# Kernel optimization log

Measured on AMD Instinct MI355X. Metric: run time of the kernel, lower is better.

## Reference

```python
import jax, jax.numpy as jnp
import numpy as np

DIM = 768
HEADS = 12
HD = DIM // HEADS
SCALE = HD ** -0.5


def setup_inputs() -> dict:
    key = jax.random.key(0)
    ks = jax.random.split(key, 12)
    B, N = 2, 2048
    s = DIM ** -0.5
    return {
        "x1": jax.random.normal(ks[0], (B, N, DIM), jnp.float32),
        "x2": jax.random.normal(ks[1], (B, N, DIM), jnp.float32),
        "Wq": jax.random.normal(ks[2], (DIM, DIM), jnp.float32) * s,
        "bq": jax.random.normal(ks[3], (DIM,), jnp.float32) * 0.01,
        "Wk": jax.random.normal(ks[4], (DIM, DIM), jnp.float32) * s,
        "bk": jax.random.normal(ks[5], (DIM,), jnp.float32) * 0.01,
        "Wv": jax.random.normal(ks[6], (DIM, DIM), jnp.float32) * s,
        "bv": jax.random.normal(ks[7], (DIM,), jnp.float32) * 0.01,
        "Wo": jax.random.normal(ks[8], (DIM, DIM), jnp.float32) * s,
        "bo": jax.random.normal(ks[9], (DIM,), jnp.float32) * 0.01,
        "cross_scale": jnp.array([0.5], jnp.float32),
    }


def _heads(x, W, b):
    # torch Linear: x @ W.T + b; then (B,N,H,hd) -> (B,H,N,hd)
    B, N, _ = x.shape
    y = x @ W.T + b
    return y.reshape(B, N, HEADS, HD).transpose(0, 2, 1, 3)


def reference(x1, x2, Wq, bq, Wk, bk, Wv, bv, Wo, bo, cross_scale):
    B, N, C = x1.shape
    q1, k1, v1 = _heads(x1, Wq, bq), _heads(x1, Wk, bk), _heads(x1, Wv, bv)
    q2, k2, v2 = _heads(x2, Wq, bq), _heads(x2, Wk, bk), _heads(x2, Wv, bv)

    s = cross_scale[0]
    attn11 = jnp.einsum('bhqd,bhkd->bhqk', q1, k1) * SCALE
    attn22 = jnp.einsum('bhqd,bhkd->bhqk', q2, k2) * SCALE
    attn12 = jnp.einsum('bhqd,bhkd->bhqk', q1, k2) * SCALE
    attn21 = jnp.einsum('bhqd,bhkd->bhqk', q2, k1) * SCALE

    a1 = jax.nn.softmax((1.0 - s) * attn11 + s * attn12, axis=-1)
    a2 = jax.nn.softmax((1.0 - s) * attn22 + s * attn21, axis=-1)

    o1 = jnp.einsum('bhqk,bhkd->bhqd', a1, v1).transpose(0, 2, 1, 3).reshape(B, N, C)
    o2 = jnp.einsum('bhqk,bhkd->bhqd', a2, v2).transpose(0, 2, 1, 3).reshape(B, N, C)

    out1 = o1 @ Wo.T + bo
    out2 = o2 @ Wo.T + bo
    return out1, out2
```

## Files before the change

kernel.cpp:

```cpp
#include <hip/hip_runtime.h>

#define KDIM 768
#define HALF 3145728
#define XAELEMS 6291456
#define WELEMS 589824
#define QS 0.18033688f

typedef __attribute__((ext_vector_type(8))) short short8;
typedef __attribute__((ext_vector_type(4))) float float4_;

__device__ __forceinline__ unsigned short f2bf(float f) {
  unsigned int u = __float_as_uint(f);
  u += 0x7fffu + ((u >> 16) & 1u);
  return (unsigned short)(u >> 16);
}

__device__ __forceinline__ void gll16(const void* g, void* l) {
  __builtin_amdgcn_global_load_lds(
      (const __attribute__((address_space(1))) unsigned int*)g,
      (__attribute__((address_space(3))) unsigned int*)l, 16, 0, 0);
}

__global__ void prep_x_kernel(const float* __restrict__ x1, const float* __restrict__ x2,
                              const float* __restrict__ cs,
                              unsigned short* __restrict__ xa, unsigned short* __restrict__ xb) {
  const int i = (blockIdx.x * 256 + threadIdx.x) * 4;
  const float s = cs[0], t_ = 1.0f - s;
  float4 a = *(const float4*)(x1 + i);
  float4 b = *(const float4*)(x2 + i);
  ushort4 ua = { f2bf(a.x), f2bf(a.y), f2bf(a.z), f2bf(a.w) };
  ushort4 ub = { f2bf(b.x), f2bf(b.y), f2bf(b.z), f2bf(b.w) };
  *(ushort4*)(xa + i) = ua;
  *(ushort4*)(xa + HALF + i) = ub;
  ushort4 c1 = { f2bf(t_*a.x + s*b.x), f2bf(t_*a.y + s*b.y), f2bf(t_*a.z + s*b.z), f2bf(t_*a.w + s*b.w) };
  ushort4 c2 = { f2bf(t_*b.x + s*a.x), f2bf(t_*b.y + s*a.y), f2bf(t_*b.z + s*a.z), f2bf(t_*b.w + s*a.w) };
  *(ushort4*)(xb + i) = c1;
  *(ushort4*)(xb + HALF + i) = c2;
}

__global__ void conv_w4_kernel(const float* __restrict__ w0, const float* __restrict__ w1,
                               const float* __restrict__ w2, const float* __restrict__ w3,
                               unsigned short* __restrict__ o0, unsigned short* __restrict__ o1,
                               unsigned short* __restrict__ o2, unsigned short* __restrict__ o3) {
  const int z = blockIdx.y;
  const float* w = (z == 0) ? w0 : (z == 1) ? w1 : (z == 2) ? w2 : w3;
  unsigned short* o = (z == 0) ? o0 : (z == 1) ? o1 : (z == 2) ? o2 : o3;
  const int i = (blockIdx.x * 256 + threadIdx.x) * 4;
  float4 a = *(const float4*)(w + i);
  ushort4 ua = { f2bf(a.x), f2bf(a.y), f2bf(a.z), f2bf(a.w) };
  *(ushort4*)(o + i) = ua;
}

__device__ __forceinline__ void gemm_mainloop(const unsigned short* __restrict__ A,
                                              const unsigned short* __restrict__ W,
                                              unsigned short* As, unsigned short* Bs,
                                              int m0, int n0, int t, float4_ (&acc)[4][4]) {
  const int lane = t & 63, quad = lane >> 4, lrow = lane & 15;
  const int wave = t >> 6;
  const int wm = (wave & 1) * 64, wn = (wave >> 1) * 64;
  for (int kt = 0; kt < KDIM; kt += 64) {
#pragma unroll
    for (int i = 0; i < 4; i++) {
      const int li = i * 256 + t;
      const int row = li >> 3, cc = (li & 7) * 8;
      gll16(A + (size_t)(m0 + row) * KDIM + kt + cc, As + li * 8);
      gll16(W + (size_t)(n0 + row) * KDIM + kt + cc, Bs + li * 8);
    }
    __syncthreads();
#pragma unroll
    for (int kk = 0; kk < 2; kk++) {
      short8 af[4], bfr[4];
#pragma unroll
      for (int i = 0; i < 4; i++)
        af[i] = *(const short8*)(As + (wm + i * 16 + lrow) * 64 + kk * 32 + quad * 8);
#pragma unroll
      for (int j = 0; j < 4; j++)
        bfr[j] = *(const short8*)(Bs + (wn + j * 16 + lrow) * 64 + kk * 32 + quad * 8);
#pragma unroll
      for (int i = 0; i < 4; i++)
#pragma unroll
        for (int j = 0; j < 4; j++)
          acc[i][j] = __builtin_amdgcn_mfma_f32_16x16x32_bf16(af[i], bfr[j], acc[i][j], 0, 0, 0);
    }
    __syncthreads();
  }
}

__global__ __launch_bounds__(256, 2)
void qkv_gemm(const unsigned short* __restrict__ xa, const unsigned short* __restrict__ xb,
              const unsigned short* __restrict__ wq, const unsigned short* __restrict__ wk,
              const unsigned short* __restrict__ wv,
              const float* __restrict__ bq, const float* __restrict__ bk, const float* __restrict__ bv,
              unsigned short* __restrict__ qo, unsigned short* __restrict__ ko,
              unsigned short* __restrict__ vto) {
  __shared__ __align__(16) unsigned short smem[16384];
  unsigned short* As = smem;
  unsigned short* Bs = smem + 8192;
  const int t = threadIdx.x;
  const int z = blockIdx.z;
  const int m0 = blockIdx.x * 128, n0 = blockIdx.y * 128;
  const unsigned short* A = (z == 1) ? xb : xa;
  const unsigned short* W = (z == 0) ? wq : (z == 1) ? wk : wv;
  const float* bias = (z == 0) ? bq : (z == 1) ? bk : bv;
  float4_ acc[4][4];
#pragma unroll
  for (int i = 0; i < 4; i++)
#pragma unroll
    for (int j = 0; j < 4; j++) acc[i][j] = (float4_){0.f, 0.f, 0.f, 0.f};
  gemm_mainloop(A, W, As, Bs, m0, n0, t, acc);

  const int lane = t & 63, quad = lane >> 4, lrow = lane & 15;
  const int wave = t >> 6;
  const int wm = (wave & 1) * 64, wn = (wave >> 1) * 64;

  if (z == 2) {
    unsigned short* Tb = smem + wave * 4096;
#pragma unroll
    for (int i = 0; i < 4; i++) {
#pragma unroll
      for (int j = 0; j < 4; j++) {
        const int nl = j * 16 + lrow;
        const float bn = bias[n0 + wn + nl];
#pragma unroll
        for (int r = 0; r < 4; r++) {
          const int ml = i * 16 + quad * 4 + r;
          const int c = ml >> 3;
          Tb[nl * 64 + ((c ^ (nl & 7)) * 8) + (ml & 7)] = f2bf(acc[i][j][r] + bn);
        }
      }
    }
    __asm__ __volatile__("s_waitcnt lgkmcnt(0)");
    const int sb = (m0 + wm) >> 11;
    const int hh = (n0 + wn) >> 6;
    const int tokbase = ((m0 + wm) & 2047);
#pragma unroll
    for (int i3 = 0; i3 < 8; i3++) {
      const int ci = i3 * 64 + lane;
      const int row = ci >> 3, p = ci & 7;
      short8 rd = *(const short8*)(Tb + row * 64 + p * 8);
      const int c = p ^ (row & 7);
      *(short8*)(vto + ((size_t)(sb * 12 + hh) * 64 + row) * 2048 + tokbase + c * 8) = rd;
    }
  } else {
    unsigned short* dst = (z == 0) ? qo : ko;
    const float scale = (z == 0) ? QS : 1.0f;
#pragma unroll
    for (int i = 0; i < 4; i++) {
#pragma unroll
      for (int j = 0; j < 4; j++) {
        const int n = n0 + wn + j * 16 + lrow;
        const float bn = bias[n];
#pragma unroll
        for (int r = 0; r < 4; r++) {
          const int m = m0 + wm + i * 16 + quad * 4 + r;
          dst[(size_t)m * KDIM + n] = f2bf((acc[i][j][r] + bn) * scale);
        }
      }
    }
  }
}

__global__ __launch_bounds__(256, 2)
void out_gemm(const unsigned short* __restrict__ ob, const unsigned short* __restrict__ wo,
              const float* __restrict__ bo, float* __restrict__ out) {
  __shared__ __align__(16) unsigned short As[128 * 64];
  __shared__ __align__(16) unsigned short Bs[128 * 64];
  const int t = threadIdx.x;
  const int m0 = blockIdx.x * 128, n0 = blockIdx.y * 128;
  float4_ acc[4][4];
#pragma unroll
  for (int i = 0; i < 4; i++)
#pragma unroll
    for (int j = 0; j < 4; j++) acc[i][j] = (float4_){0.f, 0.f, 0.f, 0.f};
  gemm_mainloop(ob, wo, As, Bs, m0, n0, t, acc);

  const int lane = t & 63, quad = lane >> 4, lrow = lane & 15;
  const int wave = t >> 6;
  const int wm = (wave & 1) * 64, wn = (wave >> 1) * 64;
#pragma unroll
  for (int i = 0; i < 4; i++) {
#pragma unroll
    for (int j = 0; j < 4; j++) {
      const int n = n0 + wn + j * 16 + lrow;
      const float bn = bo[n];
#pragma unroll
      for (int r = 0; r < 4; r++) {
        const int m = m0 + wm + i * 16 + quad * 4 + r;
        out[(size_t)m * KDIM + n] = acc[i][j][r] + bn;
      }
    }
  }
}

__global__ __launch_bounds__(256, 2)
void attn_kernel(const unsigned short* __restrict__ qg, const unsigned short* __restrict__ kg,
                 const unsigned short* __restrict__ vt, unsigned short* __restrict__ o) {
  __shared__ __align__(16) unsigned short Ks[2][64 * 64];
  __shared__ __align__(16) unsigned short Vs[2][64 * 64];
  __shared__ __align__(16) unsigned short Ps[4][32 * 72];
  const int prob = blockIdx.x >> 4;
  const int q0 = (blockIdx.x & 15) * 128;
  const int sb = prob / 12, h = prob % 12;
  const int t = threadIdx.x, w = t >> 6, lane = t & 63, quad = lane >> 4, lrow = lane & 15;
  const int mbase = sb * 2048;
  const size_t vbase = (size_t)prob * (64 * 2048);

  short8 aq[2][2];
#pragma unroll
  for (int i = 0; i < 2; i++) {
    const unsigned short* qp = qg + (size_t)(mbase + q0 + w * 32 + i * 16 + lrow) * KDIM + h * 64 + quad * 8;
    aq[i][0] = *(const short8*)qp;
    aq[i][1] = *(const short8*)(qp + 32);
  }
  float l_part[2][4] = {{0.f, 0.f, 0.f, 0.f}, {0.f, 0.f, 0.f, 0.f}};
  float4_ oa[2][4];
#pragma unroll
  for (int i = 0; i < 2; i++)
#pragma unroll
    for (int d = 0; d < 4; d++) oa[i][d] = (float4_){0.f, 0.f, 0.f, 0.f};

  auto stage = [&](int k0, int b) {
#pragma unroll
    for (int i2 = 0; i2 < 2; i2++) {
      const int li = i2 * 256 + t;
      const int row = li >> 3, p = li & 7;
      const int c = p ^ (row & 7);
      gll16(kg + (size_t)(mbase + k0 + row) * KDIM + h * 64 + c * 8, &Ks[b][li * 8]);
    }
#pragma unroll
    for (int i2 = 0; i2 < 2; i2++) {
      const int li = i2 * 256 + t;
      const int row = li >> 3, p = li & 7;
      const int c = p ^ (row & 7);
      gll16(vt + vbase + (size_t)row * 2048 + k0 + c * 8, &Vs[b][li * 8]);
    }
  };
  stage(0, 0);

  for (int kt = 0; kt < 32; kt++) {
    __syncthreads();
    const int b = kt & 1;
    if (kt + 1 < 32) stage((kt + 1) * 64, b ^ 1);

    float4_ sc[2][4];
#pragma unroll
    for (int i = 0; i < 2; i++)
#pragma unroll
      for (int nt = 0; nt < 4; nt++) sc[i][nt] = (float4_){0.f, 0.f, 0.f, 0.f};
#pragma unroll
    for (int kk = 0; kk < 2; kk++) {
#pragma unroll
      for (int nt = 0; nt < 4; nt++) {
        short8 bk_ = *(const short8*)(&Ks[b][(nt * 16 + lrow) * 64 + (((kk * 4 + quad) ^ (lrow & 7)) * 8)]);
        sc[0][nt] = __builtin_amdgcn_mfma_f32_16x16x32_bf16(aq[0][kk], bk_, sc[0][nt], 0, 0, 0);
        sc[1][nt] = __builtin_amdgcn_mfma_f32_16x16x32_bf16(aq[1][kk], bk_, sc[1][nt], 0, 0, 0);
      }
    }

    unsigned short* pw = &Ps[w][0];
#pragma unroll
    for (int i = 0; i < 2; i++)
#pragma unroll
      for (int nt = 0; nt < 4; nt++)
#pragma unroll
        for (int r = 0; r < 4; r++) {
          const float p = __builtin_amdgcn_exp2f(sc[i][nt][r]);
          l_part[i][r] += p;
          pw[(i * 16 + quad * 4 + r) * 72 + nt * 16 + lrow] = f2bf(p);
        }
    __asm__ __volatile__("s_waitcnt lgkmcnt(0)");

#pragma unroll
    for (int kk = 0; kk < 2; kk++) {
      short8 ap0 = *(const short8*)(pw + (0 * 16 + lrow) * 72 + kk * 32 + quad * 8);
      short8 ap1 = *(const short8*)(pw + (1 * 16 + lrow) * 72 + kk * 32 + quad * 8);
#pragma unroll
      for (int dt = 0; dt < 4; dt++) {
        short8 bv_ = *(const short8*)(&Vs[b][(dt * 16 + lrow) * 64 + (((kk * 4 + quad) ^ (lrow & 7)) * 8)]);
        oa[0][dt] = __builtin_amdgcn_mfma_f32_16x16x32_bf16(ap0, bv_, oa[0][dt], 0, 0, 0);
        oa[1][dt] = __builtin_amdgcn_mfma_f32_16x16x32_bf16(ap1, bv_, oa[1][dt], 0, 0, 0);
      }
    }
  }

#pragma unroll
  for (int i = 0; i < 2; i++) {
#pragma unroll
    for (int r = 0; r < 4; r++) {
      float l = l_part[i][r];
      l += __shfl_xor(l, 1);
      l += __shfl_xor(l, 2);
      l += __shfl_xor(l, 4);
      l += __shfl_xor(l, 8);
      const float inv = 1.0f / l;
      const size_t m = (size_t)mbase + q0 + w * 32 + i * 16 + quad * 4 + r;
#pragma unroll
      for (int dt = 0; dt < 4; dt++)
        o[m * KDIM + h * 64 + dt * 16 + lrow] = f2bf(oa[i][dt][r] * inv);
    }
  }
}

extern "C" void kernel_launch(void* const* d_in, const int* in_sizes, int n_in,
                              void* d_out, int out_size, void* d_ws, size_t ws_size,
                              hipStream_t stream) {
  const float* x1 = (const float*)d_in[0];
  const float* x2 = (const float*)d_in[1];
  const float* Wq = (const float*)d_in[2];
  const float* bq = (const float*)d_in[3];
  const float* Wk = (const float*)d_in[4];
  const float* bk = (const float*)d_in[5];
  const float* Wv = (const float*)d_in[6];
  const float* bv = (const float*)d_in[7];
  const float* Wo = (const float*)d_in[8];
  const float* bo = (const float*)d_in[9];
  const float* cs = (const float*)d_in[10];
  float* out = (float*)d_out;

  char* ws = (char*)d_ws;
  size_t off = 0;
  auto alloc = [&](size_t bytes) {
    void* p = ws + off;
    off += (bytes + 255) & ~(size_t)255;
    return p;
  };
  unsigned short* xa  = (unsigned short*)alloc((size_t)XAELEMS * 2);
  unsigned short* xb  = (unsigned short*)alloc((size_t)XAELEMS * 2);
  unsigned short* wqb = (unsigned short*)alloc((size_t)WELEMS * 2);
  unsigned short* wkb = (unsigned short*)alloc((size_t)WELEMS * 2);
  unsigned short* wvb = (unsigned short*)alloc((size_t)WELEMS * 2);
  unsigned short* wob = (unsigned short*)alloc((size_t)WELEMS * 2);
  unsigned short* qg  = (unsigned short*)alloc((size_t)XAELEMS * 2);
  unsigned short* kgb = (unsigned short*)alloc((size_t)XAELEMS * 2);
  unsigned short* vtb = (unsigned short*)alloc((size_t)XAELEMS * 2);
  unsigned short* ob  = (unsigned short*)alloc((size_t)XAELEMS * 2);

  prep_x_kernel<<<HALF / 1024, 256, 0, stream>>>(x1, x2, cs, xa, xb);
  conv_w4_kernel<<<dim3(WELEMS / 1024, 4), 256, 0, stream>>>(Wq, Wk, Wv, Wo, wqb, wkb, wvb, wob);
  qkv_gemm<<<dim3(64, 6, 3), 256, 0, stream>>>(xa, xb, wqb, wkb, wvb, bq, bk, bv, qg, kgb, vtb);
  attn_kernel<<<48 * 16, 256, 0, stream>>>(qg, kgb, vtb, ob);
  out_gemm<<<dim3(64, 6), 256, 0, stream>>>(ob, wob, bo, out);
}
```

Measured before the change: 241.8 us.

## Keep attention probabilities in registers via transposed MFMA, drop LDS P staging

Computes S^T by swapping the MFMA operands (K as A, Q as B), so each lane already holds P in the B-operand layout of a 16x16x16 bf16 MFMA for the PV product. This removes the per-tile LDS write and read of P and the wait between them. Row sums now reduce across quads with two shuffles, and the output is stored as packed bf16 pairs. The block index mapping also changes so that consecutive blocks walk heads first, and bf16 rounding switches to a cheaper round-half-up pack. The trade-off is twice as many smaller MFMAs for PV with 8-byte V reads.

```diff
diff --git a/kernel.cpp b/kernel.cpp
--- a/kernel.cpp
+++ b/kernel.cpp
@@ -7,7 +7,9 @@
 #define QS 0.18033688f
 
 typedef __attribute__((ext_vector_type(8))) short short8;
+typedef __attribute__((ext_vector_type(4))) short short4_;
 typedef __attribute__((ext_vector_type(4))) float float4_;
+typedef __attribute__((ext_vector_type(2))) unsigned int uint2_;
 
 __device__ __forceinline__ unsigned short f2bf(float f) {
   unsigned int u = __float_as_uint(f);
@@ -15,11 +17,29 @@
   return (unsigned short)(u >> 16);
 }
 
+__device__ __forceinline__ unsigned int pack2bf(float a, float b) {
+  unsigned int ua = __float_as_uint(a) + 0x8000u;
+  unsigned int ub = __float_as_uint(b) + 0x8000u;
+  return __builtin_amdgcn_perm(ub, ua, 0x07060302);
+}
+
 __device__ __forceinline__ void gll16(const void* g, void* l) {
   __builtin_amdgcn_global_load_lds(
       (const __attribute__((address_space(1))) unsigned int*)g,
       (__attribute__((address_space(3))) unsigned int*)l, 16, 0, 0);
 }
+
+#if __has_builtin(__builtin_amdgcn_mfma_f32_16x16x16bf16_1k)
+__device__ __forceinline__ float4_ mfma16(short4_ a, short4_ b, float4_ c) {
+  return __builtin_amdgcn_mfma_f32_16x16x16bf16_1k(a, b, c, 0, 0, 0);
+}
+#else
+__device__ __forceinline__ float4_ mfma16(short4_ a, short4_ b, float4_ c) {
+  asm volatile("v_mfma_f32_16x16x16_bf16 %0, %1, %2, %0\n\ts_nop 7\n\ts_nop 7"
+               : "+v"(c) : "v"(a), "v"(b));
+  return c;
+}
+#endif
 
 __global__ void prep_x_kernel(const float* __restrict__ x1, const float* __restrict__ x2,
                               const float* __restrict__ cs,
@@ -197,22 +217,21 @@
                  const unsigned short* __restrict__ vt, unsigned short* __restrict__ o) {
   __shared__ __align__(16) unsigned short Ks[2][64 * 64];
   __shared__ __align__(16) unsigned short Vs[2][64 * 64];
-  __shared__ __align__(16) unsigned short Ps[4][32 * 72];
-  const int prob = blockIdx.x >> 4;
-  const int q0 = (blockIdx.x & 15) * 128;
+  const int prob = blockIdx.x % 48;
+  const int q0 = (blockIdx.x / 48) * 128;
   const int sb = prob / 12, h = prob % 12;
   const int t = threadIdx.x, w = t >> 6, lane = t & 63, quad = lane >> 4, lrow = lane & 15;
   const int mbase = sb * 2048;
   const size_t vbase = (size_t)prob * (64 * 2048);
 
-  short8 aq[2][2];
+  short8 bq[2][2];
 #pragma unroll
   for (int i = 0; i < 2; i++) {
     const unsigned short* qp = qg + (size_t)(mbase + q0 + w * 32 + i * 16 + lrow) * KDIM + h * 64 + quad * 8;
-    aq[i][0] = *(const short8*)qp;
-    aq[i][1] = *(const short8*)(qp + 32);
-  }
-  float l_part[2][4] = {{0.f, 0.f, 0.f, 0.f}, {0.f, 0.f, 0.f, 0.f}};
+    bq[i][0] = *(const short8*)qp;
+    bq[i][1] = *(const short8*)(qp + 32);
+  }
+  float l_part[2] = {0.f, 0.f};
   float4_ oa[2][4];
 #pragma unroll
   for (int i = 0; i < 2; i++)
@@ -242,61 +261,59 @@
     const int b = kt & 1;
     if (kt + 1 < 32) stage((kt + 1) * 64, b ^ 1);
 
-    float4_ sc[2][4];
-#pragma unroll
-    for (int i = 0; i < 2; i++)
-#pragma unroll
-      for (int nt = 0; nt < 4; nt++) sc[i][nt] = (float4_){0.f, 0.f, 0.f, 0.f};
+    float4_ st[4][2];
+#pragma unroll
+    for (int nt = 0; nt < 4; nt++)
+#pragma unroll
+      for (int i = 0; i < 2; i++) st[nt][i] = (float4_){0.f, 0.f, 0.f, 0.f};
 #pragma unroll
     for (int kk = 0; kk < 2; kk++) {
 #pragma unroll
       for (int nt = 0; nt < 4; nt++) {
-        short8 bk_ = *(const short8*)(&Ks[b][(nt * 16 + lrow) * 64 + (((kk * 4 + quad) ^ (lrow & 7)) * 8)]);
-        sc[0][nt] = __builtin_amdgcn_mfma_f32_16x16x32_bf16(aq[0][kk], bk_, sc[0][nt], 0, 0, 0);
-        sc[1][nt] = __builtin_amdgcn_mfma_f32_16x16x32_bf16(aq[1][kk], bk_, sc[1][nt], 0, 0, 0);
-      }
-    }
-
-    unsigned short* pw = &Ps[w][0];
-#pragma unroll
-    for (int i = 0; i < 2; i++)
-#pragma unroll
-      for (int nt = 0; nt < 4; nt++)
-#pragma unroll
-        for (int r = 0; r < 4; r++) {
-          const float p = __builtin_amdgcn_exp2f(sc[i][nt][r]);
-          l_part[i][r] += p;
-          pw[(i * 16 + quad * 4 + r) * 72 + nt * 16 + lrow] = f2bf(p);
-        }
-    __asm__ __volatile__("s_waitcnt lgkmcnt(0)");
-
-#pragma unroll
-    for (int kk = 0; kk < 2; kk++) {
-      short8 ap0 = *(const short8*)(pw + (0 * 16 + lrow) * 72 + kk * 32 + quad * 8);
-      short8 ap1 = *(const short8*)(pw + (1 * 16 + lrow) * 72 + kk * 32 + quad * 8);
+        short8 ak = *(const short8*)(&Ks[b][(nt * 16 + lrow) * 64 + (((kk * 4 + quad) ^ (lrow & 7)) * 8)]);
+        st[nt][0] = __builtin_amdgcn_mfma_f32_16x16x32_bf16(ak, bq[0][kk], st[nt][0], 0, 0, 0);
+        st[nt][1] = __builtin_amdgcn_mfma_f32_16x16x32_bf16(ak, bq[1][kk], st[nt][1], 0, 0, 0);
+      }
+    }
+
+    short4_ pb[2][4];
+#pragma unroll
+    for (int nt = 0; nt < 4; nt++)
+#pragma unroll
+      for (int i = 0; i < 2; i++) {
+        const float p0 = __builtin_amdgcn_exp2f(st[nt][i][0]);
+        const float p1 = __builtin_amdgcn_exp2f(st[nt][i][1]);
+        const float p2 = __builtin_amdgcn_exp2f(st[nt][i][2]);
+        const float p3 = __builtin_amdgcn_exp2f(st[nt][i][3]);
+        l_part[i] += (p0 + p1) + (p2 + p3);
+        uint2_ uu = { pack2bf(p0, p1), pack2bf(p2, p3) };
+        pb[i][nt] = __builtin_bit_cast(short4_, uu);
+      }
+
+#pragma unroll
+    for (int nt = 0; nt < 4; nt++) {
+      const int cp = (((nt * 2 + (quad >> 1)) ^ (lrow & 7)) * 8) + (quad & 1) * 4;
 #pragma unroll
       for (int dt = 0; dt < 4; dt++) {
-        short8 bv_ = *(const short8*)(&Vs[b][(dt * 16 + lrow) * 64 + (((kk * 4 + quad) ^ (lrow & 7)) * 8)]);
-        oa[0][dt] = __builtin_amdgcn_mfma_f32_16x16x32_bf16(ap0, bv_, oa[0][dt], 0, 0, 0);
-        oa[1][dt] = __builtin_amdgcn_mfma_f32_16x16x32_bf16(ap1, bv_, oa[1][dt], 0, 0, 0);
+        short4_ av = *(const short4_*)(&Vs[b][(dt * 16 + lrow) * 64 + cp]);
+        oa[0][dt] = mfma16(av, pb[0][nt], oa[0][dt]);
+        oa[1][dt] = mfma16(av, pb[1][nt], oa[1][dt]);
       }
     }
   }
 
 #pragma unroll
   for (int i = 0; i < 2; i++) {
-#pragma unroll
-    for (int r = 0; r < 4; r++) {
-      float l = l_part[i][r];
-      l += __shfl_xor(l, 1);
-      l += __shfl_xor(l, 2);
-      l += __shfl_xor(l, 4);
-      l += __shfl_xor(l, 8);
-      const float inv = 1.0f / l;
-      const size_t m = (size_t)mbase + q0 + w * 32 + i * 16 + quad * 4 + r;
-#pragma unroll
-      for (int dt = 0; dt < 4; dt++)
-        o[m * KDIM + h * 64 + dt * 16 + lrow] = f2bf(oa[i][dt][r] * inv);
+    float l = l_part[i];
+    l += __shfl_xor(l, 16);
+    l += __shfl_xor(l, 32);
+    const float inv = 1.0f / l;
+    const size_t m = (size_t)mbase + q0 + w * 32 + i * 16 + lrow;
+#pragma unroll
+    for (int dt = 0; dt < 4; dt++) {
+      uint2_ uu = { pack2bf(oa[i][dt][0] * inv, oa[i][dt][1] * inv),
+                    pack2bf(oa[i][dt][2] * inv, oa[i][dt][3] * inv) };
+      *(uint2_*)(o + m * KDIM + h * 64 + dt * 16 + quad * 4) = uu;
     }
   }
 }
```

Result: faster. 226.6 us (-6.3%).
